# Kernel optimization log

Measured on AMD Instinct MI355X. Metric: run time of the kernel, lower is better.

The kernel has to match this reference:

```python
import jax, jax.numpy as jnp
import numpy as np

GROUP = 32          # microscale group size for both acts and weights
FP8_MAX = 448.0     # float8_e4m3fn max
FP4_TABLE = jnp.array([0.0, 0.5, 1.0, 1.5, 2.0, 3.0, 4.0, 6.0,
                       -0.0, -0.5, -1.0, -1.5, -2.0, -3.0, -4.0, -6.0], dtype=jnp.float32)


def _ue8m0_to_float(sf):
    # uint8 exponent byte placed directly into the fp32 exponent field: 2^(e-127)
    return jax.lax.bitcast_convert_type(sf.astype(jnp.uint32) << 23, jnp.float32)


def _dequant_mxfp4(w_packed, sf):
    # w_packed: [..., K//2] ints in [0,256), two e2m1 nibbles per byte (low nibble = even elem)
    lo = FP4_TABLE[w_packed & 0xF]
    hi = FP4_TABLE[(w_packed >> 4) & 0xF]
    w = jnp.stack([lo, hi], axis=-1).reshape(*w_packed.shape[:-1], -1)   # [..., K]
    s = _ue8m0_to_float(sf)                                              # [..., K//32]
    w = w.reshape(*sf.shape, GROUP) * s[..., None]
    return w.reshape(*w_packed.shape[:-1], 2 * w_packed.shape[-1])


def _quant_dequant_fp8(x):
    # Faithful to _deepseek_v4_stage_mega_moe_inputs_kernel: per-32-group amax,
    # scale = amax/448 rounded UP to a power of two (UE8M0), cast to fp8 e4m3.
    T, D = x.shape
    xg = x.reshape(T, D // GROUP, GROUP)
    amax = jnp.maximum(jnp.max(jnp.abs(xg), axis=-1), 1e-4)
    scale = amax / FP8_MAX
    bits = jax.lax.bitcast_convert_type(scale, jnp.uint32)
    exp = ((bits >> 23) & 0xFF) + ((bits & 0x7FFFFF) != 0).astype(jnp.uint32)
    exp = jnp.clip(exp, 1, 254)
    rscale = jax.lax.bitcast_convert_type(exp << 23, jnp.float32)
    q = (xg * (1.0 / rscale)[..., None]).astype(jnp.float8_e4m3fn)
    return (q.astype(jnp.float32) * rscale[..., None]).reshape(T, D)


def setup_inputs() -> dict:
    key = jax.random.key(0)
    ks = jax.random.split(key, 7)
    T, D, I, E, K = 512, 2048, 768, 16, 8
    hidden_states = jax.random.normal(ks[0], (T, D), dtype=jnp.float32)
    topk_weights = jax.random.uniform(ks[1], (T, K), dtype=jnp.float32)
    topk_weights = topk_weights / jnp.sum(topk_weights, axis=-1, keepdims=True)
    topk_ids = jax.random.randint(ks[2], (T, K), 0, E, dtype=jnp.int32)
    w13_weight = jax.random.randint(ks[3], (E, 2 * I, D // 2), 0, 256, dtype=jnp.int32)
    w13_weight_scale = jax.random.randint(ks[4], (E, 2 * I, D // GROUP), 120, 128, dtype=jnp.int32)
    w2_weight = jax.random.randint(ks[5], (E, D, I // 2), 0, 256, dtype=jnp.int32)
    w2_weight_scale = jax.random.randint(ks[6], (E, D, I // GROUP), 120, 128, dtype=jnp.int32)
    return {"hidden_states": hidden_states, "topk_weights": topk_weights,
            "topk_ids": topk_ids, "w13_weight": w13_weight,
            "w13_weight_scale": w13_weight_scale, "w2_weight": w2_weight,
            "w2_weight_scale": w2_weight_scale}


def reference(hidden_states, topk_weights, topk_ids, w13_weight, w13_weight_scale,
              w2_weight, w2_weight_scale):
    E = w13_weight.shape[0]
    I = w13_weight.shape[1] // 2
    x = _quant_dequant_fp8(hidden_states)                 # [T, D] fp8-quantized acts
    w13 = _dequant_mxfp4(w13_weight, w13_weight_scale)    # [E, 2I, D]
    w2 = _dequant_mxfp4(w2_weight, w2_weight_scale)       # [E, D, I]
    onehot = (topk_ids[:, :, None] == jnp.arange(E)[None, None, :]).astype(jnp.float32)  # [T,K,E]
    routed = jnp.any(onehot > 0, axis=1)                  # [T, E]
    Xe = routed.T[:, :, None].astype(x.dtype) * x[None]   # [E, T, D]
    h = jnp.einsum('etd,efd->etf', Xe, w13)               # [E, T, 2I]
    gate, up = h[..., :I], h[..., I:]
    a = jax.nn.silu(gate) * up                            # SiluAndMul
    ye = jnp.einsum('eti,edi->etd', a, w2)                # [E, T, D]
    comb = jnp.einsum('tke,tk->te', onehot, topk_weights) # [T, E] routing weights
    return jnp.einsum('te,etd->td', comb, ye)             # [T, D]
```

## Files before the change

kernel.cpp:

```cpp
#include <hip/hip_runtime.h>
#include <stdint.h>
#include <math.h>

#define T_TOK 512
#define DDIM  2048
#define IDIM  768
#define NEXP  16
#define TOPK  8
#define LDB   72

typedef __attribute__((ext_vector_type(8))) short bf16x8;
typedef __attribute__((ext_vector_type(4))) float f32x4;

__device__ __forceinline__ void lds_barrier() {
  asm volatile("s_waitcnt lgkmcnt(0)" ::: "memory");
  __builtin_amdgcn_s_barrier();
}

__device__ __forceinline__ float e4m3_rtne(float f) {
  uint32_t u = __float_as_uint(f);
  uint32_t sign = u & 0x80000000u;
  uint32_t a = u & 0x7FFFFFFFu;
  float fa = __uint_as_float(a);
  float out;
  if (fa >= 0.015625f) {
    uint32_t lsb = (a >> 20) & 1u;
    a += 0x0007FFFFu + lsb;
    a &= 0xFFF00000u;
    out = __uint_as_float(a);
  } else {
    out = rintf(fa * 512.0f) * 0.001953125f;
  }
  return __uint_as_float(__float_as_uint(out) | sign);
}

__global__ __launch_bounds__(512) void qdq_route_kernel(
    const float* __restrict__ x, ushort* __restrict__ xq,
    const int* __restrict__ ids, const float* __restrict__ wts,
    int* __restrict__ counts, int* __restrict__ offsets,
    short* __restrict__ lists, float* __restrict__ combs)
{
  if ((int)blockIdx.x < (int)gridDim.x - 1) {
    int idx4 = blockIdx.x * 512 + threadIdx.x;
    float4 v = ((const float4*)x)[idx4];
    float a = fmaxf(fmaxf(fabsf(v.x), fabsf(v.y)), fmaxf(fabsf(v.z), fabsf(v.w)));
#pragma unroll
    for (int m = 4; m >= 1; m >>= 1)
      a = fmaxf(a, __shfl_xor(a, m, 8));
    a = fmaxf(a, 1e-4f);
    float scale = a / 448.0f;
    uint32_t b = __float_as_uint(scale);
    uint32_t ex = ((b >> 23) & 255u) + ((b & 0x7FFFFFu) ? 1u : 0u);
    ex = ex < 1u ? 1u : (ex > 254u ? 254u : ex);
    float rscale = __uint_as_float(ex << 23);
    float inv = 1.0f / rscale;
    uint32_t r0 = __float_as_uint(e4m3_rtne(v.x * inv) * rscale) >> 16;
    uint32_t r1 = __float_as_uint(e4m3_rtne(v.y * inv) * rscale) >> 16;
    uint32_t r2 = __float_as_uint(e4m3_rtne(v.z * inv) * rscale) >> 16;
    uint32_t r3 = __float_as_uint(e4m3_rtne(v.w * inv) * rscale) >> 16;
    ((uint2*)xq)[idx4] = make_uint2(r0 | (r1 << 16), r2 | (r3 << 16));
  } else {
    __shared__ int scnt[NEXP];
    int t = threadIdx.x;
    if (t < NEXP) scnt[t] = 0;
    __syncthreads();
    int  myid[TOPK];
    float myw[TOPK];
#pragma unroll
    for (int k = 0; k < TOPK; k++) { myid[k] = ids[t*TOPK+k]; myw[k] = wts[t*TOPK+k]; }
    for (int e = 0; e < NEXP; e++) {
      float s = 0.f; bool r = false;
#pragma unroll
      for (int k = 0; k < TOPK; k++) if (myid[k] == e) { s += myw[k]; r = true; }
      if (r) {
        int slot = atomicAdd(&scnt[e], 1);
        lists[(e<<9) + slot] = (short)t;
        combs[(e<<9) + slot] = s;
      }
    }
    __syncthreads();
    if (t == 0) {
      int acc = 0;
      for (int e = 0; e < NEXP; e++) {
        offsets[e] = acc;
        int c = scnt[e];
        counts[e] = c;
        acc += c;
      }
      offsets[NEXP] = acc;
    }
  }
}

__device__ __forceinline__ void deq8(int4 w0, int4 w1, uint32_t S, ushort* dst) {
  uint32_t base = S << 6;
  uint32_t E01 = base << 16;
  uint32_t E23 = ((base + 192u) << 16) | (base + 128u);
  uint32_t E45 = ((base + 320u) << 16) | (base + 256u);
  uint32_t E67 = ((base + 448u) << 16) | (base + 384u);
  uint32_t lutLoA = __builtin_amdgcn_perm(E23, E01, 0x06040200u);
  uint32_t lutHiA = __builtin_amdgcn_perm(E23, E01, 0x07050301u);
  uint32_t lutLoB = __builtin_amdgcn_perm(E67, E45, 0x06040200u);
  uint32_t lutHiB = __builtin_amdgcn_perm(E67, E45, 0x07050301u);
  int wi[8] = {w0.x,w0.y,w0.z,w0.w, w1.x,w1.y,w1.z,w1.w};
  uint32_t od[8];
#pragma unroll
  for (int c = 0; c < 8; c += 2) {
    uint32_t a = (uint32_t)wi[c], b = (uint32_t)wi[c+1];
    uint32_t selm = ((a | (a << 4)) & 0x0707u) | ((((b | (b << 4)) & 0x0707u)) << 16);
    uint32_t sgn  = (((a << 4) | (a << 8)) & 0x8080u) | (((((b << 4) | (b << 8)) & 0x8080u)) << 16);
    uint32_t loB = __builtin_amdgcn_perm(lutLoB, lutLoA, selm);
    uint32_t hiB = __builtin_amdgcn_perm(lutHiB, lutHiA, selm) | sgn;
    od[c]   = __builtin_amdgcn_perm(hiB, loB, 0x05010400u);
    od[c+1] = __builtin_amdgcn_perm(hiB, loB, 0x07030602u);
  }
  *(uint4*)dst       = make_uint4(od[0], od[1], od[2], od[3]);
  *(uint4*)(dst + 8) = make_uint4(od[4], od[5], od[6], od[7]);
}

__global__ __launch_bounds__(256,3) void gemm1_kernel(
    const ushort* __restrict__ xq, const int* __restrict__ w13,
    const int* __restrict__ w13s, const int* __restrict__ counts,
    const int* __restrict__ offsets, const short* __restrict__ lists,
    const float* __restrict__ combs, ushort* __restrict__ a_buf)
{
  const int e  = blockIdx.x;
  const int i0 = blockIdx.y << 5;
  const int m0 = blockIdx.z << 7;
  const int cnt = counts[e];
  if (m0 >= cnt) return;
  const int NIT = DDIM / 64;

  __shared__ __align__(16) ushort Bsh[2][64*LDB];
  __shared__ int   toks[128];
  __shared__ float cmbs[128];

  const int tid = threadIdx.x;
  if (tid < 128) {
    int m = m0 + tid; bool v = m < cnt;
    toks[tid] = v ? (int)lists[(e<<9)+m] : 0;
    cmbs[tid] = v ? combs[(e<<9)+m] : 0.f;
  }
  __syncthreads();

  const int wv = tid >> 6, l = tid & 63, l16 = l & 15, q = l >> 4;

  const ushort* arow[2];
#pragma unroll
  for (int i = 0; i < 2; i++)
    arow[i] = xq + (size_t)toks[wv*32 + i*16 + l16]*DDIM + q*8;

  const int rb = tid >> 2, hq = tid & 3;
  const int feat = (rb < 32) ? (i0 + rb) : (IDIM + i0 + (rb - 32));
  const int* wrow = w13 + ((size_t)e*(2*IDIM) + feat)*(DDIM/2) + hq*8;
  const int* srow = w13s + ((size_t)e*(2*IDIM) + feat)*(DDIM/32) + (hq >> 1);
  const int bdst = rb*LDB + hq*16;

  f32x4 acc[2][4];
#pragma unroll
  for (int i = 0; i < 2; i++)
#pragma unroll
    for (int j = 0; j < 4; j++) acc[i][j] = (f32x4){0.f,0.f,0.f,0.f};

  bf16x8 aA[2][2], aB[2][2];
  int4 wA0, wA1, wB0, wB1; uint32_t SA, SB;

  {
    int4 t0 = *(const int4*)(wrow);
    int4 t1 = *(const int4*)(wrow + 4);
    uint32_t S = (((uint32_t)srow[0]) - 1u) << 1;
    deq8(t0, t1, S, &Bsh[0][bdst]);
  }
#pragma unroll
  for (int i = 0; i < 2; i++)
#pragma unroll
    for (int s = 0; s < 2; s++)
      aA[i][s] = *(const bf16x8*)(arow[i] + s*32);
  wA0 = *(const int4*)(wrow + 32); wA1 = *(const int4*)(wrow + 36);
  SA  = (((uint32_t)srow[2]) - 1u) << 1;
#pragma unroll
  for (int i = 0; i < 2; i++)
#pragma unroll
    for (int s = 0; s < 2; s++)
      aB[i][s] = *(const bf16x8*)(arow[i] + 64 + s*32);
  lds_barrier();

  for (int t = 0; t < NIT; t += 2) {
    int t2 = t + 2 < NIT ? t + 2 : NIT - 1;
    wB0 = *(const int4*)(wrow + t2*32);
    wB1 = *(const int4*)(wrow + t2*32 + 4);
    SB  = (((uint32_t)srow[t2*2]) - 1u) << 1;
#pragma unroll
    for (int s = 0; s < 2; s++) {
      bf16x8 bfr[4];
#pragma unroll
      for (int j = 0; j < 4; j++)
        bfr[j] = *(const bf16x8*)&Bsh[0][(j*16 + l16)*LDB + s*32 + q*8];
#pragma unroll
      for (int i = 0; i < 2; i++)
#pragma unroll
        for (int j = 0; j < 4; j++)
          acc[i][j] = __builtin_amdgcn_mfma_f32_16x16x32_bf16(aA[i][s], bfr[j], acc[i][j], 0, 0, 0);
    }
    deq8(wA0, wA1, SA, &Bsh[1][bdst]);
#pragma unroll
    for (int i = 0; i < 2; i++)
#pragma unroll
      for (int s = 0; s < 2; s++)
        aA[i][s] = *(const bf16x8*)(arow[i] + t2*64 + s*32);
    lds_barrier();

    int t3 = t + 3 < NIT ? t + 3 : NIT - 1;
    wA0 = *(const int4*)(wrow + t3*32);
    wA1 = *(const int4*)(wrow + t3*32 + 4);
    SA  = (((uint32_t)srow[t3*2]) - 1u) << 1;
#pragma unroll
    for (int s = 0; s < 2; s++) {
      bf16x8 bfr[4];
#pragma unroll
      for (int j = 0; j < 4; j++)
        bfr[j] = *(const bf16x8*)&Bsh[1][(j*16 + l16)*LDB + s*32 + q*8];
#pragma unroll
      for (int i = 0; i < 2; i++)
#pragma unroll
        for (int j = 0; j < 4; j++)
          acc[i][j] = __builtin_amdgcn_mfma_f32_16x16x32_bf16(aB[i][s], bfr[j], acc[i][j], 0, 0, 0);
    }
    deq8(wB0, wB1, SB, &Bsh[0][bdst]);
#pragma unroll
    for (int i = 0; i < 2; i++)
#pragma unroll
      for (int s = 0; s < 2; s++)
        aB[i][s] = *(const bf16x8*)(arow[i] + t3*64 + s*32);
    lds_barrier();
  }

  const int obase = offsets[e];
#pragma unroll
  for (int i = 0; i < 2; i++) {
#pragma unroll
    for (int r = 0; r < 4; r++) {
      int mrow = wv*32 + i*16 + q*4 + r;
      int gm = m0 + mrow;
      if (gm < cnt) {
        float c = cmbs[mrow];
        ushort* dst = a_buf + (size_t)(obase + gm)*IDIM + i0 + l16;
#pragma unroll
        for (int jj = 0; jj < 2; jj++) {
          float g = acc[i][jj][r], u = acc[i][jj+2][r];
          float val = (g / (1.f + expf(-g))) * u * c;
          uint32_t bb = __float_as_uint(val);
          bb += 0x7FFFu + ((bb >> 16) & 1u);
          dst[jj*16] = (ushort)(bb >> 16);
        }
      }
    }
  }
}

__global__ __launch_bounds__(256,4) void gemm2_kernel(
    const ushort* __restrict__ a_buf, const int* __restrict__ w2,
    const int* __restrict__ w2s, const int* __restrict__ counts,
    const int* __restrict__ offsets, const short* __restrict__ lists,
    float* __restrict__ out)
{
  const int e  = blockIdx.x;
  const int n0 = blockIdx.y << 6;
  const int m0 = blockIdx.z << 7;
  const int cnt = counts[e];
  if (m0 >= cnt) return;
  const int NIT = IDIM / 64;

  __shared__ __align__(16) ushort Bsh[2][64*LDB];

  const int tid = threadIdx.x;
  const int wv = tid >> 6, l = tid & 63, l16 = l & 15, q = l >> 4;
  const int obase = offsets[e];

  const ushort* arow[2];
#pragma unroll
  for (int i = 0; i < 2; i++) {
    int gm = m0 + wv*32 + i*16 + l16;
    int rowc = (gm < cnt) ? gm : 0;
    arow[i] = a_buf + (size_t)(obase + rowc)*IDIM + q*8;
  }

  const int rb = tid >> 2, hq = tid & 3;
  const int* wrow = w2 + ((size_t)e*DDIM + n0 + rb)*(IDIM/2) + hq*8;
  const int* srow = w2s + ((size_t)e*DDIM + n0 + rb)*(IDIM/32) + (hq >> 1);
  const int bdst = rb*LDB + hq*16;

  f32x4 acc[2][4];
#pragma unroll
  for (int i = 0; i < 2; i++)
#pragma unroll
    for (int j = 0; j < 4; j++) acc[i][j] = (f32x4){0.f,0.f,0.f,0.f};

  bf16x8 aA[2][2], aB[2][2];
  int4 wA0, wA1, wB0, wB1; uint32_t SA, SB;

  {
    int4 t0 = *(const int4*)(wrow);
    int4 t1 = *(const int4*)(wrow + 4);
    uint32_t S = (((uint32_t)srow[0]) - 1u) << 1;
    deq8(t0, t1, S, &Bsh[0][bdst]);
  }
#pragma unroll
  for (int i = 0; i < 2; i++)
#pragma unroll
    for (int s = 0; s < 2; s++)
      aA[i][s] = *(const bf16x8*)(arow[i] + s*32);
  wA0 = *(const int4*)(wrow + 32); wA1 = *(const int4*)(wrow + 36);
  SA  = (((uint32_t)srow[2]) - 1u) << 1;
#pragma unroll
  for (int i = 0; i < 2; i++)
#pragma unroll
    for (int s = 0; s < 2; s++)
      aB[i][s] = *(const bf16x8*)(arow[i] + 64 + s*32);
  lds_barrier();

  for (int t = 0; t < NIT; t += 2) {
    int t2 = t + 2 < NIT ? t + 2 : NIT - 1;
    wB0 = *(const int4*)(wrow + t2*32);
    wB1 = *(const int4*)(wrow + t2*32 + 4);
    SB  = (((uint32_t)srow[t2*2]) - 1u) << 1;
#pragma unroll
    for (int s = 0; s < 2; s++) {
      bf16x8 bfr[4];
#pragma unroll
      for (int j = 0; j < 4; j++)
        bfr[j] = *(const bf16x8*)&Bsh[0][(j*16 + l16)*LDB + s*32 + q*8];
#pragma unroll
      for (int i = 0; i < 2; i++)
#pragma unroll
        for (int j = 0; j < 4; j++)
          acc[i][j] = __builtin_amdgcn_mfma_f32_16x16x32_bf16(aA[i][s], bfr[j], acc[i][j], 0, 0, 0);
    }
    deq8(wA0, wA1, SA, &Bsh[1][bdst]);
#pragma unroll
    for (int i = 0; i < 2; i++)
#pragma unroll
      for (int s = 0; s < 2; s++)
        aA[i][s] = *(const bf16x8*)(arow[i] + t2*64 + s*32);
    lds_barrier();

    int t3 = t + 3 < NIT ? t + 3 : NIT - 1;
    wA0 = *(const int4*)(wrow + t3*32);
    wA1 = *(const int4*)(wrow + t3*32 + 4);
    SA  = (((uint32_t)srow[t3*2]) - 1u) << 1;
#pragma unroll
    for (int s = 0; s < 2; s++) {
      bf16x8 bfr[4];
#pragma unroll
      for (int j = 0; j < 4; j++)
        bfr[j] = *(const bf16x8*)&Bsh[1][(j*16 + l16)*LDB + s*32 + q*8];
#pragma unroll
      for (int i = 0; i < 2; i++)
#pragma unroll
        for (int j = 0; j < 4; j++)
          acc[i][j] = __builtin_amdgcn_mfma_f32_16x16x32_bf16(aB[i][s], bfr[j], acc[i][j], 0, 0, 0);
    }
    deq8(wB0, wB1, SB, &Bsh[0][bdst]);
#pragma unroll
    for (int i = 0; i < 2; i++)
#pragma unroll
      for (int s = 0; s < 2; s++)
        aB[i][s] = *(const bf16x8*)(arow[i] + t3*64 + s*32);
    lds_barrier();
  }

#pragma unroll
  for (int i = 0; i < 2; i++) {
#pragma unroll
    for (int r = 0; r < 4; r++) {
      int mrow = wv*32 + i*16 + q*4 + r;
      int gm = m0 + mrow;
      if (gm < cnt) {
        int tok = (int)lists[(e<<9) + gm];
        float* dst = out + (size_t)tok*DDIM + n0 + l16;
#pragma unroll
        for (int j = 0; j < 4; j++)
          atomicAdd(&dst[j*16], acc[i][j][r]);
      }
    }
  }
}

extern "C" void kernel_launch(void* const* d_in, const int* in_sizes, int n_in,
                              void* d_out, int out_size, void* d_ws, size_t ws_size,
                              hipStream_t stream)
{
  const float* x    = (const float*)d_in[0];
  const float* tw   = (const float*)d_in[1];
  const int*   tids = (const int*)d_in[2];
  const int*   w13  = (const int*)d_in[3];
  const int*   w13s = (const int*)d_in[4];
  const int*   w2   = (const int*)d_in[5];
  const int*   w2s  = (const int*)d_in[6];
  float* out = (float*)d_out;

  char* ws = (char*)d_ws;
  size_t off = 0;
  auto alloc = [&](size_t bytes) { void* p = ws + off; off = (off + bytes + 255) & ~(size_t)255; return p; };
  float* combs   = (float*)alloc((size_t)NEXP*T_TOK*4);
  short* lists   = (short*)alloc((size_t)NEXP*T_TOK*2);
  int*   counts  = (int*)alloc(64*4);
  int*   offsets = (int*)alloc(64*4);
  ushort* a_buf  = (ushort*)alloc((size_t)T_TOK*TOPK*IDIM*2);
  ushort* xq     = (ushort*)(ws + off);

  qdq_route_kernel<<<(T_TOK*DDIM)/2048 + 1, 512, 0, stream>>>(
      x, xq, tids, tw, counts, offsets, lists, combs);
  gemm1_kernel<<<dim3(NEXP, IDIM/32, 4), 256, 0, stream>>>(
      xq, w13, w13s, counts, offsets, lists, combs, a_buf);
  gemm2_kernel<<<dim3(NEXP, DDIM/64, 4), 256, 0, stream>>>(
      a_buf, w2, w2s, counts, offsets, lists, out);
}
```

Before: 290.0 us.

## Quad-buffer LDS B tiles to halve barriers and deepen weight prefetch

Both GEMM kernels now keep four LDS B buffers instead of two. Each loop iteration processes two k-steps behind a single barrier instead of two, and global weight loads are issued two k-steps further ahead. The aim is to cut barrier stalls and hide more global-load latency behind MFMA work. In exchange, LDS use per block doubles and more weight registers stay live, which may reduce occupancy under the launch bounds of 3 and 4 blocks.

```diff
diff --git a/kernel.cpp b/kernel.cpp
--- a/kernel.cpp
+++ b/kernel.cpp
@@ -131,7 +131,7 @@
   if (m0 >= cnt) return;
   const int NIT = DDIM / 64;
 
-  __shared__ __align__(16) ushort Bsh[2][64*LDB];
+  __shared__ __align__(16) ushort Bsh[4][64*LDB];
   __shared__ int   toks[128];
   __shared__ float cmbs[128];
 
@@ -163,75 +163,90 @@
     for (int j = 0; j < 4; j++) acc[i][j] = (f32x4){0.f,0.f,0.f,0.f};
 
   bf16x8 aA[2][2], aB[2][2];
-  int4 wA0, wA1, wB0, wB1; uint32_t SA, SB;
+  int4 wc00, wc01, wc10, wc11;
+  uint32_t Sc0, Sc1;
 
   {
     int4 t0 = *(const int4*)(wrow);
     int4 t1 = *(const int4*)(wrow + 4);
-    uint32_t S = (((uint32_t)srow[0]) - 1u) << 1;
-    deq8(t0, t1, S, &Bsh[0][bdst]);
-  }
+    deq8(t0, t1, (((uint32_t)srow[0]) - 1u) << 1, &Bsh[0][bdst]);
+    t0 = *(const int4*)(wrow + 32);
+    t1 = *(const int4*)(wrow + 36);
+    deq8(t0, t1, (((uint32_t)srow[2]) - 1u) << 1, &Bsh[1][bdst]);
+  }
+  wc00 = *(const int4*)(wrow + 64);  wc01 = *(const int4*)(wrow + 68);
+  Sc0  = (((uint32_t)srow[4]) - 1u) << 1;
+  wc10 = *(const int4*)(wrow + 96);  wc11 = *(const int4*)(wrow + 100);
+  Sc1  = (((uint32_t)srow[6]) - 1u) << 1;
 #pragma unroll
   for (int i = 0; i < 2; i++)
 #pragma unroll
-    for (int s = 0; s < 2; s++)
+    for (int s = 0; s < 2; s++) {
       aA[i][s] = *(const bf16x8*)(arow[i] + s*32);
-  wA0 = *(const int4*)(wrow + 32); wA1 = *(const int4*)(wrow + 36);
-  SA  = (((uint32_t)srow[2]) - 1u) << 1;
-#pragma unroll
-  for (int i = 0; i < 2; i++)
-#pragma unroll
-    for (int s = 0; s < 2; s++)
       aB[i][s] = *(const bf16x8*)(arow[i] + 64 + s*32);
+    }
   lds_barrier();
 
   for (int t = 0; t < NIT; t += 2) {
-    int t2 = t + 2 < NIT ? t + 2 : NIT - 1;
-    wB0 = *(const int4*)(wrow + t2*32);
-    wB1 = *(const int4*)(wrow + t2*32 + 4);
-    SB  = (((uint32_t)srow[t2*2]) - 1u) << 1;
+    const int idx = (t >> 1) & 1;
+    ushort* R0 = Bsh[2*idx];
+    ushort* R1 = Bsh[2*idx + 1];
+    ushort* W0 = Bsh[2 - 2*idx];
+    ushort* W1 = Bsh[3 - 2*idx];
+    int t4 = t + 4 < NIT ? t + 4 : NIT - 1;
+    int t5 = t + 5 < NIT ? t + 5 : NIT - 1;
+    int4 wn00 = *(const int4*)(wrow + t4*32);
+    int4 wn01 = *(const int4*)(wrow + t4*32 + 4);
+    uint32_t Sn0 = (((uint32_t)srow[t4*2]) - 1u) << 1;
+    int4 wn10 = *(const int4*)(wrow + t5*32);
+    int4 wn11 = *(const int4*)(wrow + t5*32 + 4);
+    uint32_t Sn1 = (((uint32_t)srow[t5*2]) - 1u) << 1;
+
 #pragma unroll
     for (int s = 0; s < 2; s++) {
       bf16x8 bfr[4];
 #pragma unroll
       for (int j = 0; j < 4; j++)
-        bfr[j] = *(const bf16x8*)&Bsh[0][(j*16 + l16)*LDB + s*32 + q*8];
+        bfr[j] = *(const bf16x8*)&R0[(j*16 + l16)*LDB + s*32 + q*8];
 #pragma unroll
       for (int i = 0; i < 2; i++)
 #pragma unroll
         for (int j = 0; j < 4; j++)
           acc[i][j] = __builtin_amdgcn_mfma_f32_16x16x32_bf16(aA[i][s], bfr[j], acc[i][j], 0, 0, 0);
     }
-    deq8(wA0, wA1, SA, &Bsh[1][bdst]);
-#pragma unroll
-    for (int i = 0; i < 2; i++)
-#pragma unroll
-      for (int s = 0; s < 2; s++)
-        aA[i][s] = *(const bf16x8*)(arow[i] + t2*64 + s*32);
-    lds_barrier();
-
-    int t3 = t + 3 < NIT ? t + 3 : NIT - 1;
-    wA0 = *(const int4*)(wrow + t3*32);
-    wA1 = *(const int4*)(wrow + t3*32 + 4);
-    SA  = (((uint32_t)srow[t3*2]) - 1u) << 1;
+    deq8(wc00, wc01, Sc0, &W0[bdst]);
+    {
+      int t2 = t + 2 < NIT ? t + 2 : NIT - 1;
+#pragma unroll
+      for (int i = 0; i < 2; i++)
+#pragma unroll
+        for (int s = 0; s < 2; s++)
+          aA[i][s] = *(const bf16x8*)(arow[i] + t2*64 + s*32);
+    }
+
 #pragma unroll
     for (int s = 0; s < 2; s++) {
       bf16x8 bfr[4];
 #pragma unroll
       for (int j = 0; j < 4; j++)
-        bfr[j] = *(const bf16x8*)&Bsh[1][(j*16 + l16)*LDB + s*32 + q*8];
+        bfr[j] = *(const bf16x8*)&R1[(j*16 + l16)*LDB + s*32 + q*8];
 #pragma unroll
       for (int i = 0; i < 2; i++)
 #pragma unroll
         for (int j = 0; j < 4; j++)
           acc[i][j] = __builtin_amdgcn_mfma_f32_16x16x32_bf16(aB[i][s], bfr[j], acc[i][j], 0, 0, 0);
     }
-    deq8(wB0, wB1, SB, &Bsh[0][bdst]);
-#pragma unroll
-    for (int i = 0; i < 2; i++)
-#pragma unroll
-      for (int s = 0; s < 2; s++)
-        aB[i][s] = *(const bf16x8*)(arow[i] + t3*64 + s*32);
+    deq8(wc10, wc11, Sc1, &W1[bdst]);
+    {
+      int t3 = t + 3 < NIT ? t + 3 : NIT - 1;
+#pragma unroll
+      for (int i = 0; i < 2; i++)
+#pragma unroll
+        for (int s = 0; s < 2; s++)
+          aB[i][s] = *(const bf16x8*)(arow[i] + t3*64 + s*32);
+    }
+    wc00 = wn00; wc01 = wn01; Sc0 = Sn0;
+    wc10 = wn10; wc11 = wn11; Sc1 = Sn1;
     lds_barrier();
   }
 
@@ -271,7 +286,7 @@
   if (m0 >= cnt) return;
   const int NIT = IDIM / 64;
 
-  __shared__ __align__(16) ushort Bsh[2][64*LDB];
+  __shared__ __align__(16) ushort Bsh[4][64*LDB];
 
   const int tid = threadIdx.x;
   const int wv = tid >> 6, l = tid & 63, l16 = l & 15, q = l >> 4;
@@ -297,75 +312,90 @@
     for (int j = 0; j < 4; j++) acc[i][j] = (f32x4){0.f,0.f,0.f,0.f};
 
   bf16x8 aA[2][2], aB[2][2];
-  int4 wA0, wA1, wB0, wB1; uint32_t SA, SB;
+  int4 wc00, wc01, wc10, wc11;
+  uint32_t Sc0, Sc1;
 
   {
     int4 t0 = *(const int4*)(wrow);
     int4 t1 = *(const int4*)(wrow + 4);
-    uint32_t S = (((uint32_t)srow[0]) - 1u) << 1;
-    deq8(t0, t1, S, &Bsh[0][bdst]);
-  }
+    deq8(t0, t1, (((uint32_t)srow[0]) - 1u) << 1, &Bsh[0][bdst]);
+    t0 = *(const int4*)(wrow + 32);
+    t1 = *(const int4*)(wrow + 36);
+    deq8(t0, t1, (((uint32_t)srow[2]) - 1u) << 1, &Bsh[1][bdst]);
+  }
+  wc00 = *(const int4*)(wrow + 64);  wc01 = *(const int4*)(wrow + 68);
+  Sc0  = (((uint32_t)srow[4]) - 1u) << 1;
+  wc10 = *(const int4*)(wrow + 96);  wc11 = *(const int4*)(wrow + 100);
+  Sc1  = (((uint32_t)srow[6]) - 1u) << 1;
 #pragma unroll
   for (int i = 0; i < 2; i++)
 #pragma unroll
-    for (int s = 0; s < 2; s++)
+    for (int s = 0; s < 2; s++) {
       aA[i][s] = *(const bf16x8*)(arow[i] + s*32);
-  wA0 = *(const int4*)(wrow + 32); wA1 = *(const int4*)(wrow + 36);
-  SA  = (((uint32_t)srow[2]) - 1u) << 1;
-#pragma unroll
-  for (int i = 0; i < 2; i++)
-#pragma unroll
-    for (int s = 0; s < 2; s++)
       aB[i][s] = *(const bf16x8*)(arow[i] + 64 + s*32);
+    }
   lds_barrier();
 
   for (int t = 0; t < NIT; t += 2) {
-    int t2 = t + 2 < NIT ? t + 2 : NIT - 1;
-    wB0 = *(const int4*)(wrow + t2*32);
-    wB1 = *(const int4*)(wrow + t2*32 + 4);
-    SB  = (((uint32_t)srow[t2*2]) - 1u) << 1;
+    const int idx = (t >> 1) & 1;
+    ushort* R0 = Bsh[2*idx];
+    ushort* R1 = Bsh[2*idx + 1];
+    ushort* W0 = Bsh[2 - 2*idx];
+    ushort* W1 = Bsh[3 - 2*idx];
+    int t4 = t + 4 < NIT ? t + 4 : NIT - 1;
+    int t5 = t + 5 < NIT ? t + 5 : NIT - 1;
+    int4 wn00 = *(const int4*)(wrow + t4*32);
+    int4 wn01 = *(const int4*)(wrow + t4*32 + 4);
+    uint32_t Sn0 = (((uint32_t)srow[t4*2]) - 1u) << 1;
+    int4 wn10 = *(const int4*)(wrow + t5*32);
+    int4 wn11 = *(const int4*)(wrow + t5*32 + 4);
+    uint32_t Sn1 = (((uint32_t)srow[t5*2]) - 1u) << 1;
+
 #pragma unroll
     for (int s = 0; s < 2; s++) {
       bf16x8 bfr[4];
 #pragma unroll
       for (int j = 0; j < 4; j++)
-        bfr[j] = *(const bf16x8*)&Bsh[0][(j*16 + l16)*LDB + s*32 + q*8];
+        bfr[j] = *(const bf16x8*)&R0[(j*16 + l16)*LDB + s*32 + q*8];
 #pragma unroll
       for (int i = 0; i < 2; i++)
 #pragma unroll
         for (int j = 0; j < 4; j++)
           acc[i][j] = __builtin_amdgcn_mfma_f32_16x16x32_bf16(aA[i][s], bfr[j], acc[i][j], 0, 0, 0);
     }
-    deq8(wA0, wA1, SA, &Bsh[1][bdst]);
-#pragma unroll
-    for (int i = 0; i < 2; i++)
-#pragma unroll
-      for (int s = 0; s < 2; s++)
-        aA[i][s] = *(const bf16x8*)(arow[i] + t2*64 + s*32);
-    lds_barrier();
-
-    int t3 = t + 3 < NIT ? t + 3 : NIT - 1;
-    wA0 = *(const int4*)(wrow + t3*32);
-    wA1 = *(const int4*)(wrow + t3*32 + 4);
-    SA  = (((uint32_t)srow[t3*2]) - 1u) << 1;
+    deq8(wc00, wc01, Sc0, &W0[bdst]);
+    {
+      int t2 = t + 2 < NIT ? t + 2 : NIT - 1;
+#pragma unroll
+      for (int i = 0; i < 2; i++)
+#pragma unroll
+        for (int s = 0; s < 2; s++)
+          aA[i][s] = *(const bf16x8*)(arow[i] + t2*64 + s*32);
+    }
+
 #pragma unroll
     for (int s = 0; s < 2; s++) {
       bf16x8 bfr[4];
 #pragma unroll
       for (int j = 0; j < 4; j++)
-        bfr[j] = *(const bf16x8*)&Bsh[1][(j*16 + l16)*LDB + s*32 + q*8];
+        bfr[j] = *(const bf16x8*)&R1[(j*16 + l16)*LDB + s*32 + q*8];
 #pragma unroll
       for (int i = 0; i < 2; i++)
 #pragma unroll
         for (int j = 0; j < 4; j++)
           acc[i][j] = __builtin_amdgcn_mfma_f32_16x16x32_bf16(aB[i][s], bfr[j], acc[i][j], 0, 0, 0);
     }
-    deq8(wB0, wB1, SB, &Bsh[0][bdst]);
-#pragma unroll
-    for (int i = 0; i < 2; i++)
-#pragma unroll
-      for (int s = 0; s < 2; s++)
-        aB[i][s] = *(const bf16x8*)(arow[i] + t3*64 + s*32);
+    deq8(wc10, wc11, Sc1, &W1[bdst]);
+    {
+      int t3 = t + 3 < NIT ? t + 3 : NIT - 1;
+#pragma unroll
+      for (int i = 0; i < 2; i++)
+#pragma unroll
+        for (int s = 0; s < 2; s++)
+          aB[i][s] = *(const bf16x8*)(arow[i] + t3*64 + s*32);
+    }
+    wc00 = wn00; wc01 = wn01; Sc0 = Sn0;
+    wc10 = wn10; wc11 = wn11; Sc1 = Sn1;
     lds_barrier();
   }
 
```

After: 277.0 us. 1.05x faster.
